# Performance work log

Measured on AMD Instinct MI355X. Metric: run time of the kernel, lower is better.

The kernel has to match this reference:

```python
import jax, jax.numpy as jnp
import numpy as np

EPS = 1e-5
CONV_THRESHOLD = 0.0


def setup_inputs() -> dict:
    key = jax.random.key(0)
    ks = jax.random.split(key, 16)
    B, F = 65536, 256
    H1, H2 = 1024, 512
    d_in = F + 1  # raw features + 1 scalar conv feature
    inp = {
        "x": jax.random.normal(ks[0], (B, F), dtype=jnp.float32),
        # layer 1: Linear(d_in, H1) + BatchNorm1d(H1)
        "W1": jax.random.normal(ks[1], (d_in, H1), dtype=jnp.float32) * (1.0 / np.sqrt(d_in)),
        "b1": jax.random.normal(ks[2], (H1,), dtype=jnp.float32) * 0.01,
        "g1": jnp.ones((H1,), jnp.float32) + 0.1 * jax.random.normal(ks[3], (H1,), dtype=jnp.float32),
        "be1": jax.random.normal(ks[4], (H1,), dtype=jnp.float32) * 0.01,
        "m1": jax.random.normal(ks[5], (H1,), dtype=jnp.float32) * 0.1,
        "v1": jax.random.uniform(ks[6], (H1,), dtype=jnp.float32, minval=0.5, maxval=1.5),
        # layer 2: Linear(H1, H2) + BatchNorm1d(H2)
        "W2": jax.random.normal(ks[7], (H1, H2), dtype=jnp.float32) * (1.0 / np.sqrt(H1)),
        "b2": jax.random.normal(ks[8], (H2,), dtype=jnp.float32) * 0.01,
        "g2": jnp.ones((H2,), jnp.float32) + 0.1 * jax.random.normal(ks[9], (H2,), dtype=jnp.float32),
        "be2": jax.random.normal(ks[10], (H2,), dtype=jnp.float32) * 0.01,
        "m2": jax.random.normal(ks[11], (H2,), dtype=jnp.float32) * 0.1,
        "v2": jax.random.uniform(ks[12], (H2,), dtype=jnp.float32, minval=0.5, maxval=1.5),
        # output head: Linear(H2, 1)
        "W3": jax.random.normal(ks[13], (H2, 1), dtype=jnp.float32) * (1.0 / np.sqrt(H2)),
        "b3": jax.random.normal(ks[14], (1,), dtype=jnp.float32) * 0.01,
    }
    return inp


def _bn(h, g, be, m, v):
    # eval-mode BatchNorm1d with running statistics
    return g * (h - m) * jax.lax.rsqrt(v + EPS) + be


def reference(x, W1, b1, g1, be1, m1, v1, W2, b2, g2, be2, m2, v2, W3, b3):
    # Batched replacement of the per-sample numpy threshold conv:
    # the Conv filter reduces the whole sample patch with a mean and thresholds it,
    # producing one binary scalar feature per sample.  [B, 1]
    conv_feat = jnp.where(jnp.mean(x, axis=1, keepdims=True) > CONV_THRESHOLD, 1.0, 0.0).astype(x.dtype)
    h = jnp.concatenate([x, conv_feat], axis=1)  # [B, F+1]
    h = jax.nn.relu(_bn(h @ W1 + b1, g1, be1, m1, v1))  # [B, H1]
    h = jax.nn.relu(_bn(h @ W2 + b2, g2, be2, m2, v2))  # [B, H2]
    return jax.nn.sigmoid(h @ W3 + b3)  # [B, 1]
```

## Files before the change

### kernel.cpp

```cpp
#include <hip/hip_runtime.h>
#include <hip/hip_bf16.h>
#include <cstdint>
#include <cstddef>

typedef __bf16 bf16_t;
typedef bf16_t bf16x8 __attribute__((ext_vector_type(8)));
typedef bf16_t bf16x4 __attribute__((ext_vector_type(4)));
typedef float f32x4 __attribute__((ext_vector_type(4)));

#define BN_EPS 1e-5f

__device__ __forceinline__ void async_load16(const bf16_t* g, bf16_t* lds) {
  __builtin_amdgcn_global_load_lds(
      (__attribute__((address_space(1))) uint32_t*)(g),
      (__attribute__((address_space(3))) uint32_t*)(lds),
      16, 0, 0);
}

__global__ void prep_all_kernel(const float* __restrict__ W1, const float* __restrict__ W2,
                                const float* b1, const float* g1, const float* be1,
                                const float* m1, const float* v1,
                                const float* b2, const float* g2, const float* be2,
                                const float* m2, const float* v2,
                                bf16_t* __restrict__ W1T, bf16_t* __restrict__ W2T,
                                float* s1, float* t1, float* s2, float* t2,
                                float* w1last) {
  const int b = blockIdx.x;
  if (b < 192) {
    const float* src;
    bf16_t* dst;
    int R, C, bx, by;
    if (b < 64) { src = W1; dst = W1T; R = 256; C = 1024; bx = b & 15; by = b >> 4; }
    else        { src = W2; dst = W2T; R = 1024; C = 512; bx = (b - 64) & 7; by = (b - 64) >> 3; }
    __shared__ bf16_t tile[64][66];
    const int r0 = by * 64, c0 = bx * 64;
    const int tc = threadIdx.x & 63;
    const int tr4 = threadIdx.x >> 6;
#pragma unroll
    for (int i = 0; i < 16; ++i) {
      int r = i * 4 + tr4;
      tile[r][tc] = (bf16_t)src[(size_t)(r0 + r) * C + c0 + tc];
    }
    __syncthreads();
#pragma unroll
    for (int i = 0; i < 16; ++i) {
      int rr = i * 4 + tr4;
      dst[(size_t)(c0 + rr) * R + r0 + tc] = tile[tc][rr];
    }
  } else {
    int i = (b - 192) * 256 + threadIdx.x;
    if (i < 1024) {
      float s = g1[i] * rsqrtf(v1[i] + BN_EPS);
      s1[i] = s;
      t1[i] = be1[i] - m1[i] * s + b1[i] * s;
      w1last[i] = W1[256 * 1024 + i];
    }
    if (i < 512) {
      float s = g2[i] * rsqrtf(v2[i] + BN_EPS);
      s2[i] = s;
      t2[i] = be2[i] - m2[i] * s + b2[i] * s;
    }
  }
}

__global__ void prep_x_kernel(const float* __restrict__ x, bf16_t* __restrict__ xb,
                              float* __restrict__ convf, float* __restrict__ outacc) {
  int lane = threadIdx.x & 63;
  int w = threadIdx.x >> 6;
  int row = blockIdx.x * 4 + w;
  const float4 v = *(const float4*)(x + (size_t)row * 256 + lane * 4);
  float s = v.x + v.y + v.z + v.w;
  bf16x4 o = {(bf16_t)v.x, (bf16_t)v.y, (bf16_t)v.z, (bf16_t)v.w};
  *(bf16x4*)(xb + (size_t)row * 256 + lane * 4) = o;
#pragma unroll
  for (int off = 32; off >= 1; off >>= 1) s += __shfl_down(s, off);
  if (lane == 0) convf[row] = (s > 0.0f) ? 1.0f : 0.0f;
  if (threadIdx.x < 4) outacc[blockIdx.x * 4 + threadIdx.x] = 0.0f;
}

template <int K>
__device__ __forceinline__ void gemm_core_256x128(
    const bf16_t* __restrict__ A, const bf16_t* __restrict__ BT,
    int mTile, int nTile, bf16_t* As, bf16_t* Bs,
    int w, int lane, f32x4 (&acc)[4][8]) {
  const int l15 = lane & 15;
  const int quad = lane >> 4;
  const int sRow = lane >> 2;
  const int sCol = (lane & 3) * 8;
  const bf16_t* gA = A + (size_t)(mTile + w * 64 + sRow) * K + sCol;
  const bf16_t* gB = BT + (size_t)(nTile + w * 32 + sRow) * K + sCol;
  bf16_t* lA = As + (w * 64) * 32;
  bf16_t* lB = Bs + (w * 32) * 32;

  for (int k0 = 0; k0 < K; k0 += 32) {
    async_load16(gA + k0, lA);
    async_load16(gA + (size_t)16 * K + k0, lA + 16 * 32);
    async_load16(gA + (size_t)32 * K + k0, lA + 32 * 32);
    async_load16(gA + (size_t)48 * K + k0, lA + 48 * 32);
    async_load16(gB + k0, lB);
    async_load16(gB + (size_t)16 * K + k0, lB + 16 * 32);
    __syncthreads();

    bf16x8 af[4], bfr[8];
#pragma unroll
    for (int t = 0; t < 4; ++t)
      af[t] = *(const bf16x8*)(As + (w * 64 + t * 16 + l15) * 32 + quad * 8);
#pragma unroll
    for (int t = 0; t < 8; ++t)
      bfr[t] = *(const bf16x8*)(Bs + (t * 16 + l15) * 32 + quad * 8);
#pragma unroll
    for (int ti = 0; ti < 4; ++ti)
#pragma unroll
      for (int tj = 0; tj < 8; ++tj)
        acc[ti][tj] = __builtin_amdgcn_mfma_f32_16x16x32_bf16(af[ti], bfr[tj], acc[ti][tj], 0, 0, 0);
    __syncthreads();
  }
}

__global__ __launch_bounds__(256, 2) void gemm1_kernel(
    const bf16_t* __restrict__ A, const bf16_t* __restrict__ BT,
    const float* __restrict__ sN, const float* __restrict__ tN,
    const float* __restrict__ convf, const float* __restrict__ w1last,
    bf16_t* __restrict__ out) {
  constexpr int K = 256, N = 1024;
  __shared__ __align__(16) bf16_t As[256 * 32];
  __shared__ __align__(16) bf16_t Bs[128 * 32];

  const int b = blockIdx.x;
  const int mTile = ((b >> 6) * 8 + (b & 7)) * 256;
  const int nTile = ((b >> 3) & 7) * 128;

  const int tid = threadIdx.x;
  const int lane = tid & 63;
  const int w = tid >> 6;
  const int l15 = lane & 15;
  const int quad = lane >> 4;

  f32x4 acc[4][8];
#pragma unroll
  for (int i = 0; i < 4; ++i)
#pragma unroll
    for (int j = 0; j < 8; ++j) {
      f32x4 z = {0.f, 0.f, 0.f, 0.f};
      acc[i][j] = z;
    }

  gemm_core_256x128<K>(A, BT, mTile, nTile, As, Bs, w, lane, acc);

  float sc[8], tc[8], wl[8];
#pragma unroll
  for (int tj = 0; tj < 8; ++tj) {
    int c = nTile + tj * 16 + l15;
    sc[tj] = sN[c];
    tc[tj] = tN[c];
    wl[tj] = w1last[c];
  }
#pragma unroll
  for (int ti = 0; ti < 4; ++ti)
#pragma unroll
    for (int r = 0; r < 4; ++r) {
      int row = mTile + w * 64 + ti * 16 + quad * 4 + r;
      float cf = convf[row];
      size_t base = (size_t)row * N + nTile;
#pragma unroll
      for (int tj = 0; tj < 8; ++tj) {
        float z = acc[ti][tj][r] + cf * wl[tj];
        z = fmaxf(z * sc[tj] + tc[tj], 0.f);
        out[base + tj * 16 + l15] = (bf16_t)z;
      }
    }
}

__global__ __launch_bounds__(256, 2) void gemm2_head_kernel(
    const bf16_t* __restrict__ A, const bf16_t* __restrict__ BT,
    const float* __restrict__ sN, const float* __restrict__ tN,
    const float* __restrict__ W3, float* __restrict__ outacc) {
  constexpr int K = 1024;
  __shared__ __align__(16) bf16_t As[256 * 32];
  __shared__ __align__(16) bf16_t Bs[128 * 32];

  const int b = blockIdx.x;
  const int mTile = ((b >> 5) * 8 + (b & 7)) * 256;
  const int nTile = ((b >> 3) & 3) * 128;

  const int tid = threadIdx.x;
  const int lane = tid & 63;
  const int w = tid >> 6;
  const int l15 = lane & 15;
  const int quad = lane >> 4;

  f32x4 acc[4][8];
#pragma unroll
  for (int i = 0; i < 4; ++i)
#pragma unroll
    for (int j = 0; j < 8; ++j) {
      f32x4 z = {0.f, 0.f, 0.f, 0.f};
      acc[i][j] = z;
    }

  gemm_core_256x128<K>(A, BT, mTile, nTile, As, Bs, w, lane, acc);

  float sc[8], tc[8], w3c[8];
#pragma unroll
  for (int tj = 0; tj < 8; ++tj) {
    int c = nTile + tj * 16 + l15;
    sc[tj] = sN[c];
    tc[tj] = tN[c];
    w3c[tj] = W3[c];
  }
#pragma unroll
  for (int ti = 0; ti < 4; ++ti)
#pragma unroll
    for (int r = 0; r < 4; ++r) {
      float p = 0.f;
#pragma unroll
      for (int tj = 0; tj < 8; ++tj) {
        float z = fmaxf(acc[ti][tj][r] * sc[tj] + tc[tj], 0.f);
        p += z * w3c[tj];
      }
#pragma unroll
      for (int m = 1; m <= 8; m <<= 1) p += __shfl_xor(p, m);
      if (l15 == 0)
        atomicAdd(outacc + mTile + w * 64 + ti * 16 + quad * 4 + r, p);
    }
}

__global__ void sigmoid_kernel(float* __restrict__ out, const float* __restrict__ b3) {
  int i = blockIdx.x * 256 + threadIdx.x;
  float z = out[i] + b3[0];
  out[i] = 1.0f / (1.0f + expf(-z));
}

extern "C" void kernel_launch(void* const* d_in, const int* in_sizes, int n_in,
                              void* d_out, int out_size, void* d_ws, size_t ws_size,
                              hipStream_t stream) {
  const float* x = (const float*)d_in[0];
  const float* W1 = (const float*)d_in[1];
  const float* b1 = (const float*)d_in[2];
  const float* g1 = (const float*)d_in[3];
  const float* be1 = (const float*)d_in[4];
  const float* m1 = (const float*)d_in[5];
  const float* v1 = (const float*)d_in[6];
  const float* W2 = (const float*)d_in[7];
  const float* b2 = (const float*)d_in[8];
  const float* g2 = (const float*)d_in[9];
  const float* be2 = (const float*)d_in[10];
  const float* m2 = (const float*)d_in[11];
  const float* v2 = (const float*)d_in[12];
  const float* W3 = (const float*)d_in[13];
  const float* b3 = (const float*)d_in[14];
  float* out = (float*)d_out;

  char* p = (char*)d_ws;
  bf16_t* h1 = (bf16_t*)p;    p += (size_t)65536 * 1024 * 2;
  bf16_t* xb = (bf16_t*)p;    p += (size_t)65536 * 256 * 2;
  bf16_t* W1T = (bf16_t*)p;   p += (size_t)1024 * 256 * 2;
  bf16_t* W2T = (bf16_t*)p;   p += (size_t)512 * 1024 * 2;
  float* convf = (float*)p;   p += (size_t)65536 * 4;
  float* w1last = (float*)p;  p += 1024 * 4;
  float* s1 = (float*)p;      p += 1024 * 4;
  float* t1 = (float*)p;      p += 1024 * 4;
  float* s2 = (float*)p;      p += 512 * 4;
  float* t2 = (float*)p;      p += 512 * 4;

  prep_all_kernel<<<196, 256, 0, stream>>>(W1, W2, b1, g1, be1, m1, v1,
                                           b2, g2, be2, m2, v2,
                                           W1T, W2T, s1, t1, s2, t2, w1last);
  prep_x_kernel<<<16384, 256, 0, stream>>>(x, xb, convf, out);

  gemm1_kernel<<<2048, 256, 0, stream>>>(xb, W1T, s1, t1, convf, w1last, h1);
  gemm2_head_kernel<<<1024, 256, 0, stream>>>(h1, W2T, s2, t2, W3, out);

  sigmoid_kernel<<<256, 256, 0, stream>>>(out, b3);
}
```

Before: 256.5 us.

## Use BK=64 with XOR-swizzled LDS, merge prep kernels, fuse sigmoid via last-block counter

The GEMM core now stages 64-wide K slices instead of 32, with an XOR swizzle on the LDS column chunks. This halves the number of barrier pairs per tile and is meant to avoid LDS bank conflicts on fragment reads. The two prep kernels are merged into one launch, and the sigmoid kernel is removed: the last of the four N-tile blocks for each M tile, found through an atomic counter, applies the bias and sigmoid. In exchange, LDS use per block doubles (48KB at two blocks per CU), and the change adds counter atomics and fences.

Result: slower. 280.1 us (+9.2%).

```diff
diff --git a/kernel.cpp b/kernel.cpp
--- a/kernel.cpp
+++ b/kernel.cpp
@@ -17,16 +17,31 @@
       16, 0, 0);
 }
 
-__global__ void prep_all_kernel(const float* __restrict__ W1, const float* __restrict__ W2,
-                                const float* b1, const float* g1, const float* be1,
-                                const float* m1, const float* v1,
-                                const float* b2, const float* g2, const float* be2,
-                                const float* m2, const float* v2,
-                                bf16_t* __restrict__ W1T, bf16_t* __restrict__ W2T,
-                                float* s1, float* t1, float* s2, float* t2,
-                                float* w1last) {
-  const int b = blockIdx.x;
-  if (b < 192) {
+__global__ void prep_kernel(const float* __restrict__ x, bf16_t* __restrict__ xb,
+                            float* __restrict__ convf, float* __restrict__ outacc,
+                            const float* __restrict__ W1, const float* __restrict__ W2,
+                            const float* b1, const float* g1, const float* be1,
+                            const float* m1, const float* v1,
+                            const float* b2, const float* g2, const float* be2,
+                            const float* m2, const float* v2,
+                            bf16_t* __restrict__ W1T, bf16_t* __restrict__ W2T,
+                            float* s1, float* t1, float* s2, float* t2,
+                            float* w1last, unsigned int* cnt) {
+  const int blk = blockIdx.x;
+  if (blk < 16384) {
+    int lane = threadIdx.x & 63;
+    int w = threadIdx.x >> 6;
+    int row = blk * 4 + w;
+    const float4 v = *(const float4*)(x + (size_t)row * 256 + lane * 4);
+    float s = v.x + v.y + v.z + v.w;
+    bf16x4 o = {(bf16_t)v.x, (bf16_t)v.y, (bf16_t)v.z, (bf16_t)v.w};
+    *(bf16x4*)(xb + (size_t)row * 256 + lane * 4) = o;
+#pragma unroll
+    for (int off = 32; off >= 1; off >>= 1) s += __shfl_down(s, off);
+    if (lane == 0) convf[row] = (s > 0.0f) ? 1.0f : 0.0f;
+    if (threadIdx.x < 4) outacc[blk * 4 + threadIdx.x] = 0.0f;
+  } else if (blk < 16576) {
+    const int b = blk - 16384;
     const float* src;
     bf16_t* dst;
     int R, C, bx, by;
@@ -48,7 +63,7 @@
       dst[(size_t)(c0 + rr) * R + r0 + tc] = tile[tc][rr];
     }
   } else {
-    int i = (b - 192) * 256 + threadIdx.x;
+    int i = (blk - 16576) * 256 + threadIdx.x;
     if (i < 1024) {
       float s = g1[i] * rsqrtf(v1[i] + BN_EPS);
       s1[i] = s;
@@ -60,22 +75,8 @@
       s2[i] = s;
       t2[i] = be2[i] - m2[i] * s + b2[i] * s;
     }
-  }
-}
-
-__global__ void prep_x_kernel(const float* __restrict__ x, bf16_t* __restrict__ xb,
-                              float* __restrict__ convf, float* __restrict__ outacc) {
-  int lane = threadIdx.x & 63;
-  int w = threadIdx.x >> 6;
-  int row = blockIdx.x * 4 + w;
-  const float4 v = *(const float4*)(x + (size_t)row * 256 + lane * 4);
-  float s = v.x + v.y + v.z + v.w;
-  bf16x4 o = {(bf16_t)v.x, (bf16_t)v.y, (bf16_t)v.z, (bf16_t)v.w};
-  *(bf16x4*)(xb + (size_t)row * 256 + lane * 4) = o;
-#pragma unroll
-  for (int off = 32; off >= 1; off >>= 1) s += __shfl_down(s, off);
-  if (lane == 0) convf[row] = (s > 0.0f) ? 1.0f : 0.0f;
-  if (threadIdx.x < 4) outacc[blockIdx.x * 4 + threadIdx.x] = 0.0f;
+    if (i < 256) cnt[i] = 0u;
+  }
 }
 
 template <int K>
@@ -85,34 +86,38 @@
     int w, int lane, f32x4 (&acc)[4][8]) {
   const int l15 = lane & 15;
   const int quad = lane >> 4;
-  const int sRow = lane >> 2;
-  const int sCol = (lane & 3) * 8;
-  const bf16_t* gA = A + (size_t)(mTile + w * 64 + sRow) * K + sCol;
-  const bf16_t* gB = BT + (size_t)(nTile + w * 32 + sRow) * K + sCol;
-  bf16_t* lA = As + (w * 64) * 32;
-  bf16_t* lB = Bs + (w * 32) * 32;
-
-  for (int k0 = 0; k0 < K; k0 += 32) {
-    async_load16(gA + k0, lA);
-    async_load16(gA + (size_t)16 * K + k0, lA + 16 * 32);
-    async_load16(gA + (size_t)32 * K + k0, lA + 32 * 32);
-    async_load16(gA + (size_t)48 * K + k0, lA + 48 * 32);
-    async_load16(gB + k0, lB);
-    async_load16(gB + (size_t)16 * K + k0, lB + 16 * 32);
+  const int r8 = lane >> 3;
+  const int c8 = (lane & 7) ^ r8;
+  const int swz = l15 & 7;
+  const bf16_t* gA = A + (size_t)(mTile + w * 64 + r8) * K + c8 * 8;
+  const bf16_t* gB = BT + (size_t)(nTile + w * 32 + r8) * K + c8 * 8;
+  bf16_t* lA = As + (w * 64) * 64;
+  bf16_t* lB = Bs + (w * 32) * 64;
+
+  for (int k0 = 0; k0 < K; k0 += 64) {
+#pragma unroll
+    for (int i = 0; i < 8; ++i)
+      async_load16(gA + (size_t)(i * 8) * K + k0, lA + (i * 8) * 64);
+#pragma unroll
+    for (int i = 0; i < 4; ++i)
+      async_load16(gB + (size_t)(i * 8) * K + k0, lB + (i * 8) * 64);
     __syncthreads();
 
-    bf16x8 af[4], bfr[8];
-#pragma unroll
-    for (int t = 0; t < 4; ++t)
-      af[t] = *(const bf16x8*)(As + (w * 64 + t * 16 + l15) * 32 + quad * 8);
-#pragma unroll
-    for (int t = 0; t < 8; ++t)
-      bfr[t] = *(const bf16x8*)(Bs + (t * 16 + l15) * 32 + quad * 8);
-#pragma unroll
-    for (int ti = 0; ti < 4; ++ti)
-#pragma unroll
-      for (int tj = 0; tj < 8; ++tj)
-        acc[ti][tj] = __builtin_amdgcn_mfma_f32_16x16x32_bf16(af[ti], bfr[tj], acc[ti][tj], 0, 0, 0);
+#pragma unroll
+    for (int kk = 0; kk < 2; ++kk) {
+      bf16x8 af[4], bfr[8];
+#pragma unroll
+      for (int t = 0; t < 4; ++t)
+        af[t] = *(const bf16x8*)(As + (w * 64 + t * 16 + l15) * 64 + ((kk * 4 + quad) ^ swz) * 8);
+#pragma unroll
+      for (int t = 0; t < 8; ++t)
+        bfr[t] = *(const bf16x8*)(Bs + (t * 16 + l15) * 64 + ((kk * 4 + quad) ^ swz) * 8);
+#pragma unroll
+      for (int ti = 0; ti < 4; ++ti)
+#pragma unroll
+        for (int tj = 0; tj < 8; ++tj)
+          acc[ti][tj] = __builtin_amdgcn_mfma_f32_16x16x32_bf16(af[ti], bfr[tj], acc[ti][tj], 0, 0, 0);
+    }
     __syncthreads();
   }
 }
@@ -123,8 +128,8 @@
     const float* __restrict__ convf, const float* __restrict__ w1last,
     bf16_t* __restrict__ out) {
   constexpr int K = 256, N = 1024;
-  __shared__ __align__(16) bf16_t As[256 * 32];
-  __shared__ __align__(16) bf16_t Bs[128 * 32];
+  __shared__ __align__(16) bf16_t As[256 * 64];
+  __shared__ __align__(16) bf16_t Bs[128 * 64];
 
   const int b = blockIdx.x;
   const int mTile = ((b >> 6) * 8 + (b & 7)) * 256;
@@ -174,13 +179,16 @@
 __global__ __launch_bounds__(256, 2) void gemm2_head_kernel(
     const bf16_t* __restrict__ A, const bf16_t* __restrict__ BT,
     const float* __restrict__ sN, const float* __restrict__ tN,
-    const float* __restrict__ W3, float* __restrict__ outacc) {
+    const float* __restrict__ W3, const float* __restrict__ b3,
+    float* __restrict__ outacc, unsigned int* __restrict__ cnt) {
   constexpr int K = 1024;
-  __shared__ __align__(16) bf16_t As[256 * 32];
-  __shared__ __align__(16) bf16_t Bs[128 * 32];
+  __shared__ __align__(16) bf16_t As[256 * 64];
+  __shared__ __align__(16) bf16_t Bs[128 * 64];
+  __shared__ int isLast;
 
   const int b = blockIdx.x;
-  const int mTile = ((b >> 5) * 8 + (b & 7)) * 256;
+  const int mt = (b >> 5) * 8 + (b & 7);
+  const int mTile = mt * 256;
   const int nTile = ((b >> 3) & 3) * 128;
 
   const int tid = threadIdx.x;
@@ -223,12 +231,20 @@
       if (l15 == 0)
         atomicAdd(outacc + mTile + w * 64 + ti * 16 + quad * 4 + r, p);
     }
-}
-
-__global__ void sigmoid_kernel(float* __restrict__ out, const float* __restrict__ b3) {
-  int i = blockIdx.x * 256 + threadIdx.x;
-  float z = out[i] + b3[0];
-  out[i] = 1.0f / (1.0f + expf(-z));
+
+  __syncthreads();
+  if (tid == 0) {
+    __threadfence();
+    unsigned int old = atomicAdd(&cnt[mt], 1u);
+    isLast = (old == 3u) ? 1 : 0;
+  }
+  __syncthreads();
+  if (isLast) {
+    __threadfence();
+    float z = __hip_atomic_load(&outacc[mTile + tid], __ATOMIC_RELAXED,
+                                __HIP_MEMORY_SCOPE_AGENT) + b3[0];
+    outacc[mTile + tid] = 1.0f / (1.0f + expf(-z));
+  }
 }
 
 extern "C" void kernel_launch(void* const* d_in, const int* in_sizes, int n_in,
@@ -262,14 +278,13 @@
   float* t1 = (float*)p;      p += 1024 * 4;
   float* s2 = (float*)p;      p += 512 * 4;
   float* t2 = (float*)p;      p += 512 * 4;
-
-  prep_all_kernel<<<196, 256, 0, stream>>>(W1, W2, b1, g1, be1, m1, v1,
-                                           b2, g2, be2, m2, v2,
-                                           W1T, W2T, s1, t1, s2, t2, w1last);
-  prep_x_kernel<<<16384, 256, 0, stream>>>(x, xb, convf, out);
+  unsigned int* cnt = (unsigned int*)p;  p += 256 * 4;
+
+  prep_kernel<<<16580, 256, 0, stream>>>(x, xb, convf, out,
+                                         W1, W2, b1, g1, be1, m1, v1,
+                                         b2, g2, be2, m2, v2,
+                                         W1T, W2T, s1, t1, s2, t2, w1last, cnt);
 
   gemm1_kernel<<<2048, 256, 0, stream>>>(xb, W1T, s1, t1, convf, w1last, h1);
-  gemm2_head_kernel<<<1024, 256, 0, stream>>>(h1, W2T, s2, t2, W3, out);
-
-  sigmoid_kernel<<<256, 256, 0, stream>>>(out, b3);
-}
+  gemm2_head_kernel<<<1024, 256, 0, stream>>>(h1, W2T, s2, t2, W3, b3, out, cnt);
+}
```

## Keep full gemm1 A tile resident in LDS and merge prep kernels

Applied to the files above, without the earlier changes.

gemm1 now loads a 128x256 row block of xb once into a swizzled LDS buffer. Each block then sweeps all 1024 output columns, streaming W1T in 32-wide K slices, rather than reloading A for every 128-column tile across 2048 blocks. The two prep kernels are also fused into a single launch to save one launch and its gap. In exchange, gemm1 uses much more LDS per block, B loads are not double-buffered so each slice waits on two barriers, and the grid shrinks to 512 blocks, which may limit latency hiding.

Result: no change. 259.1 us (+1.0%).

```diff
diff --git a/kernel.cpp b/kernel.cpp
--- a/kernel.cpp
+++ b/kernel.cpp
@@ -17,16 +17,31 @@
       16, 0, 0);
 }
 
-__global__ void prep_all_kernel(const float* __restrict__ W1, const float* __restrict__ W2,
-                                const float* b1, const float* g1, const float* be1,
-                                const float* m1, const float* v1,
-                                const float* b2, const float* g2, const float* be2,
-                                const float* m2, const float* v2,
-                                bf16_t* __restrict__ W1T, bf16_t* __restrict__ W2T,
-                                float* s1, float* t1, float* s2, float* t2,
-                                float* w1last) {
-  const int b = blockIdx.x;
-  if (b < 192) {
+__global__ void prep_kernel(const float* __restrict__ x, bf16_t* __restrict__ xb,
+                            float* __restrict__ convf, float* __restrict__ outacc,
+                            const float* __restrict__ W1, const float* __restrict__ W2,
+                            const float* b1, const float* g1, const float* be1,
+                            const float* m1, const float* v1,
+                            const float* b2, const float* g2, const float* be2,
+                            const float* m2, const float* v2,
+                            bf16_t* __restrict__ W1T, bf16_t* __restrict__ W2T,
+                            float* s1, float* t1, float* s2, float* t2,
+                            float* w1last) {
+  const int blk = blockIdx.x;
+  if (blk < 16384) {
+    int lane = threadIdx.x & 63;
+    int w = threadIdx.x >> 6;
+    int row = blk * 4 + w;
+    const float4 v = *(const float4*)(x + (size_t)row * 256 + lane * 4);
+    float s = v.x + v.y + v.z + v.w;
+    bf16x4 o = {(bf16_t)v.x, (bf16_t)v.y, (bf16_t)v.z, (bf16_t)v.w};
+    *(bf16x4*)(xb + (size_t)row * 256 + lane * 4) = o;
+#pragma unroll
+    for (int off = 32; off >= 1; off >>= 1) s += __shfl_down(s, off);
+    if (lane == 0) convf[row] = (s > 0.0f) ? 1.0f : 0.0f;
+    if (threadIdx.x < 4) outacc[blk * 4 + threadIdx.x] = 0.0f;
+  } else if (blk < 16576) {
+    const int b = blk - 16384;
     const float* src;
     bf16_t* dst;
     int R, C, bx, by;
@@ -48,7 +63,7 @@
       dst[(size_t)(c0 + rr) * R + r0 + tc] = tile[tc][rr];
     }
   } else {
-    int i = (b - 192) * 256 + threadIdx.x;
+    int i = (blk - 16576) * 256 + threadIdx.x;
     if (i < 1024) {
       float s = g1[i] * rsqrtf(v1[i] + BN_EPS);
       s1[i] = s;
@@ -63,34 +78,131 @@
   }
 }
 
-__global__ void prep_x_kernel(const float* __restrict__ x, bf16_t* __restrict__ xb,
-                              float* __restrict__ convf, float* __restrict__ outacc) {
-  int lane = threadIdx.x & 63;
-  int w = threadIdx.x >> 6;
-  int row = blockIdx.x * 4 + w;
-  const float4 v = *(const float4*)(x + (size_t)row * 256 + lane * 4);
-  float s = v.x + v.y + v.z + v.w;
-  bf16x4 o = {(bf16_t)v.x, (bf16_t)v.y, (bf16_t)v.z, (bf16_t)v.w};
-  *(bf16x4*)(xb + (size_t)row * 256 + lane * 4) = o;
-#pragma unroll
-  for (int off = 32; off >= 1; off >>= 1) s += __shfl_down(s, off);
-  if (lane == 0) convf[row] = (s > 0.0f) ? 1.0f : 0.0f;
-  if (threadIdx.x < 4) outacc[blockIdx.x * 4 + threadIdx.x] = 0.0f;
-}
-
-template <int K>
-__device__ __forceinline__ void gemm_core_256x128(
+__global__ __launch_bounds__(256, 2) void gemm1_kernel(
+    const bf16_t* __restrict__ xb, const bf16_t* __restrict__ W1T,
+    const float* __restrict__ s1, const float* __restrict__ t1,
+    const float* __restrict__ convf, const float* __restrict__ w1last,
+    bf16_t* __restrict__ h1) {
+  __shared__ __align__(16) bf16_t As[128 * 256];
+  __shared__ __align__(16) bf16_t Bs[2][128 * 32];
+
+  const int tid = threadIdx.x;
+  const int lane = tid & 63;
+  const int w = tid >> 6;
+  const int p = w >> 1;
+  const int h = w & 1;
+  const int l15 = lane & 15;
+  const int quad = lane >> 4;
+  const int mTile = blockIdx.x * 128;
+
+  {
+    const int rsub = lane >> 5;
+    const int c = lane & 31;
+#pragma unroll
+    for (int i = 0; i < 16; ++i) {
+      int row = w * 32 + i * 2 + rsub;
+      bf16x8 v = *(const bf16x8*)(xb + (size_t)(mTile + row) * 256 + c * 8);
+      *(bf16x8*)&As[row * 256 + (c ^ (row & 7)) * 8] = v;
+    }
+  }
+
+  const float b3dummy = 0.f; (void)b3dummy;
+
+  for (int j = 0; j < 4; ++j) {
+    const int colbase = (p * 4 + j) * 128;
+    f32x4 acc[4][8];
+#pragma unroll
+    for (int i = 0; i < 4; ++i)
+#pragma unroll
+      for (int t = 0; t < 8; ++t) {
+        f32x4 z = {0.f, 0.f, 0.f, 0.f};
+        acc[i][t] = z;
+      }
+
+    const bf16_t* gB = W1T + (size_t)(colbase + h * 64 + (lane >> 2)) * 256 + (lane & 3) * 8;
+    bf16_t* lB = Bs[p] + (h * 64) * 32;
+
+    for (int ks = 0; ks < 8; ++ks) {
+      __syncthreads();
+#pragma unroll
+      for (int i = 0; i < 4; ++i)
+        async_load16(gB + (size_t)(i * 16) * 256 + ks * 32, lB + (i * 16) * 32);
+      __syncthreads();
+
+      bf16x8 af[4], bfr[8];
+#pragma unroll
+      for (int ti = 0; ti < 4; ++ti) {
+        int row = h * 64 + ti * 16 + l15;
+        af[ti] = *(const bf16x8*)&As[row * 256 + ((ks * 4 + quad) ^ (l15 & 7)) * 8];
+      }
+#pragma unroll
+      for (int tj = 0; tj < 8; ++tj)
+        bfr[tj] = *(const bf16x8*)(Bs[p] + (tj * 16 + l15) * 32 + quad * 8);
+#pragma unroll
+      for (int ti = 0; ti < 4; ++ti)
+#pragma unroll
+        for (int tj = 0; tj < 8; ++tj)
+          acc[ti][tj] = __builtin_amdgcn_mfma_f32_16x16x32_bf16(af[ti], bfr[tj], acc[ti][tj], 0, 0, 0);
+    }
+
+    float sc[8], tc[8], wl[8];
+#pragma unroll
+    for (int tj = 0; tj < 8; ++tj) {
+      int c = colbase + tj * 16 + l15;
+      sc[tj] = s1[c];
+      tc[tj] = t1[c];
+      wl[tj] = w1last[c];
+    }
+#pragma unroll
+    for (int ti = 0; ti < 4; ++ti)
+#pragma unroll
+      for (int r = 0; r < 4; ++r) {
+        int row = mTile + h * 64 + ti * 16 + quad * 4 + r;
+        float cf = convf[row];
+        size_t base = (size_t)row * 1024 + colbase;
+#pragma unroll
+        for (int tj = 0; tj < 8; ++tj) {
+          float z = acc[ti][tj][r] + cf * wl[tj];
+          z = fmaxf(z * sc[tj] + tc[tj], 0.f);
+          h1[base + tj * 16 + l15] = (bf16_t)z;
+        }
+      }
+  }
+}
+
+__global__ __launch_bounds__(256, 2) void gemm2_head_kernel(
     const bf16_t* __restrict__ A, const bf16_t* __restrict__ BT,
-    int mTile, int nTile, bf16_t* As, bf16_t* Bs,
-    int w, int lane, f32x4 (&acc)[4][8]) {
+    const float* __restrict__ sN, const float* __restrict__ tN,
+    const float* __restrict__ W3, float* __restrict__ outacc) {
+  constexpr int K = 1024;
+  __shared__ __align__(16) bf16_t As[256 * 32];
+  __shared__ __align__(16) bf16_t Bs[128 * 32];
+
+  const int b = blockIdx.x;
+  const int mTile = ((b >> 5) * 8 + (b & 7)) * 256;
+  const int nTile = ((b >> 3) & 3) * 128;
+
+  const int tid = threadIdx.x;
+  const int lane = tid & 63;
+  const int w = tid >> 6;
   const int l15 = lane & 15;
   const int quad = lane >> 4;
   const int sRow = lane >> 2;
   const int sCol = (lane & 3) * 8;
+
   const bf16_t* gA = A + (size_t)(mTile + w * 64 + sRow) * K + sCol;
   const bf16_t* gB = BT + (size_t)(nTile + w * 32 + sRow) * K + sCol;
   bf16_t* lA = As + (w * 64) * 32;
   bf16_t* lB = Bs + (w * 32) * 32;
+
+  f32x4 acc[4][8];
+#pragma unroll
+  for (int i = 0; i < 4; ++i)
+#pragma unroll
+    for (int j = 0; j < 8; ++j) {
+      f32x4 z = {0.f, 0.f, 0.f, 0.f};
+      acc[i][j] = z;
+    }
 
   for (int k0 = 0; k0 < K; k0 += 32) {
     async_load16(gA + k0, lA);
@@ -115,90 +227,6 @@
         acc[ti][tj] = __builtin_amdgcn_mfma_f32_16x16x32_bf16(af[ti], bfr[tj], acc[ti][tj], 0, 0, 0);
     __syncthreads();
   }
-}
-
-__global__ __launch_bounds__(256, 2) void gemm1_kernel(
-    const bf16_t* __restrict__ A, const bf16_t* __restrict__ BT,
-    const float* __restrict__ sN, const float* __restrict__ tN,
-    const float* __restrict__ convf, const float* __restrict__ w1last,
-    bf16_t* __restrict__ out) {
-  constexpr int K = 256, N = 1024;
-  __shared__ __align__(16) bf16_t As[256 * 32];
-  __shared__ __align__(16) bf16_t Bs[128 * 32];
-
-  const int b = blockIdx.x;
-  const int mTile = ((b >> 6) * 8 + (b & 7)) * 256;
-  const int nTile = ((b >> 3) & 7) * 128;
-
-  const int tid = threadIdx.x;
-  const int lane = tid & 63;
-  const int w = tid >> 6;
-  const int l15 = lane & 15;
-  const int quad = lane >> 4;
-
-  f32x4 acc[4][8];
-#pragma unroll
-  for (int i = 0; i < 4; ++i)
-#pragma unroll
-    for (int j = 0; j < 8; ++j) {
-      f32x4 z = {0.f, 0.f, 0.f, 0.f};
-      acc[i][j] = z;
-    }
-
-  gemm_core_256x128<K>(A, BT, mTile, nTile, As, Bs, w, lane, acc);
-
-  float sc[8], tc[8], wl[8];
-#pragma unroll
-  for (int tj = 0; tj < 8; ++tj) {
-    int c = nTile + tj * 16 + l15;
-    sc[tj] = sN[c];
-    tc[tj] = tN[c];
-    wl[tj] = w1last[c];
-  }
-#pragma unroll
-  for (int ti = 0; ti < 4; ++ti)
-#pragma unroll
-    for (int r = 0; r < 4; ++r) {
-      int row = mTile + w * 64 + ti * 16 + quad * 4 + r;
-      float cf = convf[row];
-      size_t base = (size_t)row * N + nTile;
-#pragma unroll
-      for (int tj = 0; tj < 8; ++tj) {
-        float z = acc[ti][tj][r] + cf * wl[tj];
-        z = fmaxf(z * sc[tj] + tc[tj], 0.f);
-        out[base + tj * 16 + l15] = (bf16_t)z;
-      }
-    }
-}
-
-__global__ __launch_bounds__(256, 2) void gemm2_head_kernel(
-    const bf16_t* __restrict__ A, const bf16_t* __restrict__ BT,
-    const float* __restrict__ sN, const float* __restrict__ tN,
-    const float* __restrict__ W3, float* __restrict__ outacc) {
-  constexpr int K = 1024;
-  __shared__ __align__(16) bf16_t As[256 * 32];
-  __shared__ __align__(16) bf16_t Bs[128 * 32];
-
-  const int b = blockIdx.x;
-  const int mTile = ((b >> 5) * 8 + (b & 7)) * 256;
-  const int nTile = ((b >> 3) & 3) * 128;
-
-  const int tid = threadIdx.x;
-  const int lane = tid & 63;
-  const int w = tid >> 6;
-  const int l15 = lane & 15;
-  const int quad = lane >> 4;
-
-  f32x4 acc[4][8];
-#pragma unroll
-  for (int i = 0; i < 4; ++i)
-#pragma unroll
-    for (int j = 0; j < 8; ++j) {
-      f32x4 z = {0.f, 0.f, 0.f, 0.f};
-      acc[i][j] = z;
-    }
-
-  gemm_core_256x128<K>(A, BT, mTile, nTile, As, Bs, w, lane, acc);
 
   float sc[8], tc[8], w3c[8];
 #pragma unroll
@@ -263,12 +291,12 @@
   float* s2 = (float*)p;      p += 512 * 4;
   float* t2 = (float*)p;      p += 512 * 4;
 
-  prep_all_kernel<<<196, 256, 0, stream>>>(W1, W2, b1, g1, be1, m1, v1,
-                                           b2, g2, be2, m2, v2,
-                                           W1T, W2T, s1, t1, s2, t2, w1last);
-  prep_x_kernel<<<16384, 256, 0, stream>>>(x, xb, convf, out);
-
-  gemm1_kernel<<<2048, 256, 0, stream>>>(xb, W1T, s1, t1, convf, w1last, h1);
+  prep_kernel<<<16580, 256, 0, stream>>>(x, xb, convf, out,
+                                         W1, W2, b1, g1, be1, m1, v1,
+                                         b2, g2, be2, m2, v2,
+                                         W1T, W2T, s1, t1, s2, t2, w1last);
+
+  gemm1_kernel<<<512, 256, 0, stream>>>(xb, W1T, s1, t1, convf, w1last, h1);
   gemm2_head_kernel<<<1024, 256, 0, stream>>>(h1, W2T, s2, t2, W3, out);
 
   sigmoid_kernel<<<256, 256, 0, stream>>>(out, b3);
```
